# Optimization experiments

Hardware: AMD Instinct MI355X
Metric: run time of the kernel (lower is better)

Reference implementation:

```python
import jax, jax.numpy as jnp
import numpy as np

N = 100000   # nodes
E = 640000   # edges
D = 128      # hidden/in channels
G = 64       # graphs in batch
L = 3        # GCN layers (n_layers - 1)
EPS = 1e-5   # batchnorm eps


def _bn(h, gamma, beta):
    # BatchNorm1d in train mode: biased variance over the node axis
    m = h.mean(axis=0)
    v = h.var(axis=0)
    return (h - m) * jax.lax.rsqrt(v + EPS) * gamma + beta


def setup_inputs() -> dict:
    key = jax.random.key(0)
    ks = jax.random.split(key, 20)
    s = 1.0 / np.sqrt(D)
    inp = {
        "x": jax.random.normal(ks[0], (N, D), jnp.float32),
        "edge_index": jax.random.randint(ks[1], (2, E), 0, N, dtype=jnp.int64),
        "batch": jnp.sort(jax.random.randint(ks[2], (N,), 0, G, dtype=jnp.int64)),
        # encoder MLP (2 layers, batchnorm+relu between)
        "enc_W1": jax.random.normal(ks[3], (D, D), jnp.float32) * s,
        "enc_b1": jnp.zeros((D,), jnp.float32),
        "enc_g": jnp.ones((D,), jnp.float32),
        "enc_be": jnp.zeros((D,), jnp.float32),
        "enc_W2": jax.random.normal(ks[4], (D, D), jnp.float32) * s,
        "enc_b2": jnp.zeros((D,), jnp.float32),
        # stacked GCN layer params
        "conv_W": jax.random.normal(ks[5], (L, D, D), jnp.float32) * s,
        "conv_b": jnp.zeros((L, D), jnp.float32),
        "bn_g": jnp.ones((L, D), jnp.float32),
        "bn_b": jnp.zeros((L, D), jnp.float32),
        # MLPReadout: 128 -> 64 -> 32 -> 1
        "ro_W1": jax.random.normal(ks[6], (D, D // 2), jnp.float32) * s,
        "ro_b1": jnp.zeros((D // 2,), jnp.float32),
        "ro_W2": jax.random.normal(ks[7], (D // 2, D // 4), jnp.float32) * (1.0 / np.sqrt(D // 2)),
        "ro_b2": jnp.zeros((D // 4,), jnp.float32),
        "ro_W3": jax.random.normal(ks[8], (D // 4, 1), jnp.float32) * (1.0 / np.sqrt(D // 4)),
        "ro_b3": jnp.zeros((1,), jnp.float32),
    }
    return inp


def reference(x, edge_index, batch, enc_W1, enc_b1, enc_g, enc_be, enc_W2, enc_b2,
              conv_W, conv_b, bn_g, bn_b, ro_W1, ro_b1, ro_W2, ro_b2, ro_W3, ro_b3):
    src, dst = edge_index[0], edge_index[1]

    # gcn_norm (add_self_loops=False): deg from target column, sym normalization
    deg = jax.ops.segment_sum(jnp.ones((E,), x.dtype), dst, num_segments=N)
    dinv = jnp.where(deg > 0, jax.lax.rsqrt(jnp.maximum(deg, 1.0)), 0.0)
    norm = (dinv[src] * dinv[dst])[:, None]  # [E,1]

    # encoder MLP: Linear -> BN -> ReLU -> Linear
    h = jax.nn.relu(_bn(x @ enc_W1 + enc_b1, enc_g, enc_be))
    h = h @ enc_W2 + enc_b2

    # stacked GCN layers with BN + ReLU + residual
    for l in range(L):
        hw = h @ conv_W[l]                         # [N,D]
        agg = jax.ops.segment_sum(hw[src] * norm, dst, num_segments=N)
        agg = agg + conv_b[l]
        h = h + jax.nn.relu(_bn(agg, bn_g[l], bn_b[l]))

    # scatter-sum pooling per graph
    hg = jax.ops.segment_sum(h, batch, num_segments=G)  # [G,D]

    # MLP readout
    y = jax.nn.relu(hg @ ro_W1 + ro_b1)
    y = jax.nn.relu(y @ ro_W2 + ro_b2)
    y = y @ ro_W3 + ro_b3
    return y
```

## Files before the change

kernel.cpp:

```cpp
#include <hip/hip_runtime.h>
#include <hip/hip_bf16.h>

#define NN 100000
#define NE 640000
#define DD 128
#define NG 64
#define NL 3
#define BN_EPS 1e-5f

typedef unsigned short u16;
typedef unsigned int u32;
typedef __attribute__((ext_vector_type(8))) short short8;
typedef __attribute__((ext_vector_type(4))) float f32x4;

__device__ __forceinline__ void atomAddG(float* p, float v) { unsafeAtomicAdd(p, v); }

__device__ __forceinline__ float bf_lo(u32 u) { return __uint_as_float(u << 16); }
__device__ __forceinline__ float bf_hi(u32 u) { return __uint_as_float(u & 0xffff0000u); }
__device__ __forceinline__ float bfs(short s) { return __uint_as_float(((u32)(u16)s) << 16); }
__device__ __forceinline__ u16 bfb(float f) {
    __hip_bfloat16 b = __float2bfloat16(f);
    return *(u16*)&b;
}
__device__ __forceinline__ u32 pk(float a, float b) {
    return (u32)bfb(a) | ((u32)bfb(b) << 16);
}

__global__ void k_degI(const int* __restrict__ dst, int* __restrict__ degI) {
    int e = blockIdx.x * 256 + threadIdx.x;
    if (e < NE) atomicAdd(&degI[dst[e]], 1);
}

__global__ void k_dinv(const int* __restrict__ degI, float* __restrict__ dinv) {
    int i = blockIdx.x * 256 + threadIdx.x;
    if (i < NN) { int d = degI[i]; dinv[i] = d > 0 ? rsqrtf((float)d) : 0.f; }
}

__global__ void k_scan1(const int* __restrict__ degI, int* __restrict__ offs, int* __restrict__ bsum) {
    __shared__ int ls[256];
    int t = threadIdx.x;
    int i = blockIdx.x * 256 + t;
    int v = (i < NN) ? degI[i] : 0;
    ls[t] = v;
    __syncthreads();
    for (int off = 1; off < 256; off <<= 1) {
        int u = (t >= off) ? ls[t - off] : 0;
        __syncthreads();
        ls[t] += u;
        __syncthreads();
    }
    if (i < NN) offs[i] = ls[t] - v;
    if (t == 255) bsum[blockIdx.x] = ls[255];
}

__global__ void k_scan2(int* __restrict__ bsum, int nb) {
    __shared__ int ls[512];
    int t = threadIdx.x;
    int v = (t < nb) ? bsum[t] : 0;
    ls[t] = v;
    __syncthreads();
    for (int off = 1; off < 512; off <<= 1) {
        int u = (t >= off) ? ls[t - off] : 0;
        __syncthreads();
        ls[t] += u;
        __syncthreads();
    }
    if (t < nb) bsum[t] = ls[t] - v;
}

__global__ void k_scan3(int* __restrict__ offs, const int* __restrict__ bsum) {
    int i = blockIdx.x * 256 + threadIdx.x;
    if (i < NN) offs[i] += bsum[blockIdx.x];
    if (i == 0) offs[NN] = NE;
}

__global__ void k_place(const int* __restrict__ src, const int* __restrict__ dst,
                        const int* __restrict__ offs, int* __restrict__ cur,
                        u32* __restrict__ eIdx) {
    int e = blockIdx.x * 256 + threadIdx.x;
    if (e < NE) {
        int d = dst[e];
        int pos = offs[d] + atomicAdd(&cur[d], 1);
        eIdx[pos] = (u32)src[e];
    }
}

__global__ void k_prepW(const float* __restrict__ W1, const float* __restrict__ W2,
                        const float* __restrict__ CW, u16* __restrict__ wtb) {
    int m = blockIdx.x >> 3;
    const float* src = (m == 0) ? W1 : (m == 1) ? W2 : CW + (size_t)(m - 2) * 16384;
    u16* dst = wtb + (size_t)m * 16384;
    int base = (blockIdx.x & 7) * 2048 + threadIdx.x;
#pragma unroll
    for (int i = 0; i < 8; ++i) {
        int idx = base + i * 256;
        int k = idx >> 7, n = idx & 127;
        dst[n * 128 + k] = bfb(src[idx]);
    }
}

template <int MODE>
__global__ __launch_bounds__(256) void k_mm(
    const void* __restrict__ Av, const u16* __restrict__ Wt,
    const float* __restrict__ bias, const float* __restrict__ scl, const float* __restrict__ shf,
    const float* __restrict__ dinv,
    u16* __restrict__ Cb, float* __restrict__ Cf,
    float* __restrict__ sSum, float* __restrict__ sSq)
{
    __shared__ float lC[64 * 128];
    int tid = threadIdx.x;
    int l = tid & 63, w = tid >> 6;
    int lr = l & 15, lg = l >> 4;
    int wcol = (w & 1) * 64, wrow = (w >> 1) * 32;

    short8 Bf[4][4];
#pragma unroll
    for (int ct = 0; ct < 4; ++ct)
#pragma unroll
        for (int ks = 0; ks < 4; ++ks)
            Bf[ct][ks] = *(const short8*)(Wt + (size_t)(wcol + ct * 16 + lr) * 128 + ks * 32 + lg * 8);

    f32x4 acc[2][4];
#pragma unroll
    for (int rg = 0; rg < 2; ++rg)
#pragma unroll
        for (int ct = 0; ct < 4; ++ct)
            acc[rg][ct] = (f32x4){0.f, 0.f, 0.f, 0.f};

    int rbase = blockIdx.x * 64 + wrow;
#pragma unroll
    for (int rg = 0; rg < 2; ++rg) {
        int row = rbase + rg * 16 + lr;
        row = min(row, NN - 1);
        short8 Af[4];
        if (MODE == 1) {
            const float* af = (const float*)Av + (size_t)row * 128 + lg * 8;
#pragma unroll
            for (int ks = 0; ks < 4; ++ks) {
                float4 v0 = *(const float4*)(af + ks * 32);
                float4 v1 = *(const float4*)(af + ks * 32 + 4);
                short8 o;
                o[0] = (short)bfb(v0.x); o[1] = (short)bfb(v0.y);
                o[2] = (short)bfb(v0.z); o[3] = (short)bfb(v0.w);
                o[4] = (short)bfb(v1.x); o[5] = (short)bfb(v1.y);
                o[6] = (short)bfb(v1.z); o[7] = (short)bfb(v1.w);
                Af[ks] = o;
            }
        } else {
            const u16* ap = (const u16*)Av + (size_t)row * 128 + lg * 8;
#pragma unroll
            for (int ks = 0; ks < 4; ++ks) Af[ks] = *(const short8*)(ap + ks * 32);
            if (MODE == 2) {
#pragma unroll
                for (int ks = 0; ks < 4; ++ks) {
                    int cb = ks * 32 + lg * 8;
                    float4 s0 = *(const float4*)(scl + cb), s1 = *(const float4*)(scl + cb + 4);
                    float4 f0 = *(const float4*)(shf + cb), f1 = *(const float4*)(shf + cb + 4);
                    short8 a = Af[ks], o;
                    o[0] = (short)bfb(fmaxf(0.f, bfs(a[0]) * s0.x + f0.x));
                    o[1] = (short)bfb(fmaxf(0.f, bfs(a[1]) * s0.y + f0.y));
                    o[2] = (short)bfb(fmaxf(0.f, bfs(a[2]) * s0.z + f0.z));
                    o[3] = (short)bfb(fmaxf(0.f, bfs(a[3]) * s0.w + f0.w));
                    o[4] = (short)bfb(fmaxf(0.f, bfs(a[4]) * s1.x + f1.x));
                    o[5] = (short)bfb(fmaxf(0.f, bfs(a[5]) * s1.y + f1.y));
                    o[6] = (short)bfb(fmaxf(0.f, bfs(a[6]) * s1.z + f1.z));
                    o[7] = (short)bfb(fmaxf(0.f, bfs(a[7]) * s1.w + f1.w));
                    Af[ks] = o;
                }
            }
        }
#pragma unroll
        for (int ks = 0; ks < 4; ++ks)
#pragma unroll
            for (int ct = 0; ct < 4; ++ct)
                acc[rg][ct] = __builtin_amdgcn_mfma_f32_16x16x32_bf16(Af[ks], Bf[ct][ks], acc[rg][ct], 0, 0, 0);
    }

    if (MODE == 2) {
#pragma unroll
        for (int ct = 0; ct < 4; ++ct) {
            float bc = bias[wcol + ct * 16 + lr];
#pragma unroll
            for (int rg = 0; rg < 2; ++rg)
#pragma unroll
                for (int j = 0; j < 4; ++j) acc[rg][ct][j] += bc;
        }
    }

#pragma unroll
    for (int rg = 0; rg < 2; ++rg)
#pragma unroll
        for (int ct = 0; ct < 4; ++ct)
#pragma unroll
            for (int j = 0; j < 4; ++j)
                lC[(wrow + rg * 16 + lg * 4 + j) * 128 + wcol + ct * 16 + lr] = acc[rg][ct][j];
    __syncthreads();

    float cs[4] = {0.f, 0.f, 0.f, 0.f}, cq[4] = {0.f, 0.f, 0.f, 0.f};
#pragma unroll
    for (int i = 0; i < 8; ++i) {
        int eidx = i * 1024 + tid * 4;
        int lrow = eidx >> 7;
        int col = eidx & 127;
        int grow = blockIdx.x * 64 + lrow;
        if (grow < NN) {
            float4 v = *(float4*)(lC + eidx);
            if (MODE == 0) {
                float dd = dinv[grow];
                v.x *= dd; v.y *= dd; v.z *= dd; v.w *= dd;
            }
            uint2 o = make_uint2(pk(v.x, v.y), pk(v.z, v.w));
            if (MODE == 0) {
                u32* Cs = (u32*)Cb;
                *(uint2*)(Cs + (size_t)grow * 64 + (col >> 1)) = o;
            } else {
                *(uint2*)(Cb + (size_t)grow * 128 + col) = o;
            }
            if (MODE == 2) *(float4*)(Cf + (size_t)grow * 128 + col) = v;
            if (MODE == 1) {
                cs[0] += v.x; cs[1] += v.y; cs[2] += v.z; cs[3] += v.w;
                cq[0] += v.x * v.x; cq[1] += v.y * v.y; cq[2] += v.z * v.z; cq[3] += v.w * v.w;
            }
        }
    }

    if (MODE == 1) {
        __syncthreads();
        int g = tid >> 5, c0 = (tid & 31) * 4;
#pragma unroll
        for (int cc = 0; cc < 4; ++cc) {
            lC[g * 128 + c0 + cc] = cs[cc];
            lC[1024 + g * 128 + c0 + cc] = cq[cc];
        }
        __syncthreads();
        if (tid < 128) {
            float s = 0.f, q = 0.f;
#pragma unroll
            for (int g2 = 0; g2 < 8; ++g2) { s += lC[g2 * 128 + tid]; q += lC[1024 + g2 * 128 + tid]; }
            atomAddG(&sSum[tid], s);
            atomAddG(&sSq[tid], q);
        }
    }
}

__global__ void k_bnfinal(const float* __restrict__ sSum, const float* __restrict__ sSq,
                          const float* __restrict__ g, const float* __restrict__ be,
                          float* __restrict__ scl, float* __restrict__ shf) {
    int c = threadIdx.x;
    float m = sSum[c] * (1.0f / NN);
    float v = sSq[c] * (1.0f / NN) - m * m;
    float s = g[c] * rsqrtf(v + BN_EPS);
    scl[c] = s;
    shf[c] = be[c] - m * s;
}

__global__ __launch_bounds__(256) void k_agg(
    const u32* __restrict__ hwb,
    const u32* __restrict__ eIdx, const int* __restrict__ offs,
    const float* __restrict__ dinv,
    u32* __restrict__ aggb, float* __restrict__ sSum, float* __restrict__ sSq)
{
    int tid = threadIdx.x;
    int lane = tid & 63;
    int wav = tid >> 6;
    int gw = blockIdx.x * 4 + wav;
    int nw = gridDim.x * 4;
    float sx0 = 0.f, sx1 = 0.f, sq0 = 0.f, sq1 = 0.f;

    for (int d0 = gw * 2; d0 < NN; d0 += nw * 2) {
        int a0 = offs[d0], a1 = offs[d0 + 1], a2 = offs[d0 + 2];
        int len0 = a1 - a0, len1 = a2 - a1;
        int m0 = max(len0 - 1, 0), m1 = max(len1 - 1, 0);
        float x0 = 0.f, y0 = 0.f, x1 = 0.f, y1 = 0.f;
        int mx = max(len0, len1);
        for (int jb = 0; jb < mx; jb += 8) {
            u32 i0[8], i1[8];
#pragma unroll
            for (int q = 0; q < 8; ++q) {
                i0[q] = eIdx[min(a0 + min(jb + q, m0), NE - 1)];
                i1[q] = eIdx[min(a1 + min(jb + q, m1), NE - 1)];
            }
            u32 u0[8], u1[8];
#pragma unroll
            for (int q = 0; q < 8; ++q) {
                u0[q] = hwb[(size_t)i0[q] * 64 + lane];
                u1[q] = hwb[(size_t)i1[q] * 64 + lane];
            }
#pragma unroll
            for (int q = 0; q < 8; ++q) {
                bool v0 = (jb + q) < len0, v1 = (jb + q) < len1;
                x0 += v0 ? bf_lo(u0[q]) : 0.f;
                y0 += v0 ? bf_hi(u0[q]) : 0.f;
                x1 += v1 ? bf_lo(u1[q]) : 0.f;
                y1 += v1 ? bf_hi(u1[q]) : 0.f;
            }
        }
        float dd0 = dinv[d0], dd1 = dinv[d0 + 1];
        x0 *= dd0; y0 *= dd0; x1 *= dd1; y1 *= dd1;
        aggb[(size_t)d0 * 64 + lane] = pk(x0, y0);
        aggb[(size_t)(d0 + 1) * 64 + lane] = pk(x1, y1);
        sx0 += x0 + x1; sx1 += y0 + y1;
        sq0 += x0 * x0 + x1 * x1; sq1 += y0 * y0 + y1 * y1;
    }

    __shared__ float ls[512], lq[512];
    ls[wav * 128 + lane * 2] = sx0;
    ls[wav * 128 + lane * 2 + 1] = sx1;
    lq[wav * 128 + lane * 2] = sq0;
    lq[wav * 128 + lane * 2 + 1] = sq1;
    __syncthreads();
    if (tid < 128) {
        float s = ls[tid] + ls[tid + 128] + ls[tid + 256] + ls[tid + 384];
        float q = lq[tid] + lq[tid + 128] + lq[tid + 256] + lq[tid + 384];
        atomAddG(&sSum[tid], s);
        atomAddG(&sSq[tid], q);
    }
}

__global__ __launch_bounds__(256) void k_update(
    float* __restrict__ h, const u32* __restrict__ aggb,
    const float* __restrict__ scl, const float* __restrict__ shf,
    u32* __restrict__ hb)
{
    int i = blockIdx.x * 256 + threadIdx.x;
    int c0 = (i * 4) & 127;
    uint2 a = *(const uint2*)(aggb + (size_t)i * 2);
    float4 hv = *(float4*)(h + (size_t)i * 4);
    float4 sv = *(const float4*)(scl + c0);
    float4 fv = *(const float4*)(shf + c0);
    hv.x += fmaxf(0.f, bf_lo(a.x) * sv.x + fv.x);
    hv.y += fmaxf(0.f, bf_hi(a.x) * sv.y + fv.y);
    hv.z += fmaxf(0.f, bf_lo(a.y) * sv.z + fv.z);
    hv.w += fmaxf(0.f, bf_hi(a.y) * sv.w + fv.w);
    *(float4*)(h + (size_t)i * 4) = hv;
    *(uint2*)(hb + (size_t)i * 2) = make_uint2(pk(hv.x, hv.y), pk(hv.z, hv.w));
}

__global__ __launch_bounds__(256) void k_pool(
    const float* __restrict__ h, const u32* __restrict__ aggb,
    const float* __restrict__ scl, const float* __restrict__ shf,
    const int* __restrict__ batch, float* __restrict__ hg)
{
    __shared__ float lsum[128];
    int tid = threadIdx.x;
    int c = tid & 127, half = tid >> 7;
    float sc = scl[c], sf = shf[c];
    int r0 = blockIdx.x * 64;
    int rend = min(r0 + 64, NN);
    int b0 = batch[r0], b1 = batch[rend - 1];

    if (b0 == b1) {
        float acc = 0.f;
        for (int r = r0 + half; r < rend; r += 2) {
            u32 a = aggb[(size_t)r * 64 + (c >> 1)];
            float av = (c & 1) ? bf_hi(a) : bf_lo(a);
            acc += h[(size_t)r * 128 + c] + fmaxf(0.f, av * sc + sf);
        }
        if (half) lsum[c] = acc;
        __syncthreads();
        if (!half) atomAddG(&hg[b0 * DD + c], acc + lsum[c]);
    } else {
        float acc = 0.f;
        int cur = batch[r0 + half];
        for (int r = r0 + half; r < rend; r += 2) {
            int b = batch[r];
            if (b != cur) { atomAddG(&hg[cur * DD + c], acc); acc = 0.f; cur = b; }
            u32 a = aggb[(size_t)r * 64 + (c >> 1)];
            float av = (c & 1) ? bf_hi(a) : bf_lo(a);
            acc += h[(size_t)r * 128 + c] + fmaxf(0.f, av * sc + sf);
        }
        atomAddG(&hg[cur * DD + c], acc);
    }
}

__global__ __launch_bounds__(128) void k_readout(
    const float* __restrict__ hg,
    const float* __restrict__ W1, const float* __restrict__ b1,
    const float* __restrict__ W2, const float* __restrict__ b2,
    const float* __restrict__ W3, const float* __restrict__ b3,
    float* __restrict__ out) {
    __shared__ float a0[128], a1[64], a2[32];
    int g = blockIdx.x, t = threadIdx.x;
    a0[t] = hg[g * DD + t];
    __syncthreads();
    if (t < 64) {
        float s = b1[t];
        for (int k = 0; k < 128; ++k) s += a0[k] * W1[k * 64 + t];
        a1[t] = fmaxf(s, 0.f);
    }
    __syncthreads();
    if (t < 32) {
        float s = b2[t];
        for (int k = 0; k < 64; ++k) s += a1[k] * W2[k * 32 + t];
        a2[t] = fmaxf(s, 0.f);
    }
    __syncthreads();
    if (t == 0) {
        float s = b3[0];
        for (int k = 0; k < 32; ++k) s += a2[k] * W3[k];
        out[g] = s;
    }
}

extern "C" void kernel_launch(void* const* d_in, const int* in_sizes, int n_in,
                              void* d_out, int out_size, void* d_ws, size_t ws_size,
                              hipStream_t stream) {
    const float* x      = (const float*)d_in[0];
    const int*   ei     = (const int*)d_in[1];
    const int*   batch  = (const int*)d_in[2];
    const float* enc_W1 = (const float*)d_in[3];
    const float* enc_g  = (const float*)d_in[5];
    const float* enc_be = (const float*)d_in[6];
    const float* enc_W2 = (const float*)d_in[7];
    const float* enc_b2 = (const float*)d_in[8];
    const float* conv_W = (const float*)d_in[9];
    const float* bn_g   = (const float*)d_in[11];
    const float* bn_b   = (const float*)d_in[12];
    const float* ro_W1  = (const float*)d_in[13];
    const float* ro_b1  = (const float*)d_in[14];
    const float* ro_W2  = (const float*)d_in[15];
    const float* ro_b2  = (const float*)d_in[16];
    const float* ro_W3  = (const float*)d_in[17];
    const float* ro_b3  = (const float*)d_in[18];

    const int* srcI = ei;
    const int* dstI = ei + NE;

    float* ws   = (float*)d_ws;
    float* h    = ws;
    u32*   aggb = (u32*)(ws + 12800000);
    u32*   hb   = (u32*)(ws + 19200000);
    u32*   t1b  = (u32*)(ws + 25600000);
    u16*   wtb  = (u16*)(ws + 32000000);
    float* dinv = ws + 32050000;
    float* sSum = ws + 32150000;
    float* sSq  = sSum + 128;
    float* scl  = sSum + 256;
    float* shf  = sSum + 384;
    float* hg   = ws + 32150512;
    int*   offs = (int*)(ws + 32160000);
    int*   degI = (int*)(ws + 32270000);
    int*   bsum = (int*)(ws + 32370000);
    u32*   eIdx = (u32*)(ws + 32380000);

    u16* tb16 = (u16*)aggb;

    k_prepW<<<40, 256, 0, stream>>>(enc_W1, enc_W2, conv_W, wtb);

    hipMemsetAsync(degI, 0, NN * sizeof(int), stream);
    k_degI<<<2500, 256, 0, stream>>>(dstI, degI);
    k_dinv<<<391, 256, 0, stream>>>(degI, dinv);
    k_scan1<<<391, 256, 0, stream>>>(degI, offs, bsum);
    k_scan2<<<1, 512, 0, stream>>>(bsum, 391);
    k_scan3<<<391, 256, 0, stream>>>(offs, bsum);
    hipMemsetAsync(degI, 0, NN * sizeof(int), stream);
    k_place<<<2500, 256, 0, stream>>>(srcI, dstI, offs, degI, eIdx);

    hipMemsetAsync(sSum, 0, 256 * sizeof(float), stream);
    k_mm<1><<<1563, 256, 0, stream>>>(x, wtb, nullptr, nullptr, nullptr, nullptr, tb16, nullptr, sSum, sSq);
    k_bnfinal<<<1, 128, 0, stream>>>(sSum, sSq, enc_g, enc_be, scl, shf);
    k_mm<2><<<1563, 256, 0, stream>>>(tb16, wtb + 16384, enc_b2, scl, shf, nullptr, (u16*)hb, h, nullptr, nullptr);

    for (int l = 0; l < NL; ++l) {
        k_mm<0><<<1563, 256, 0, stream>>>((const u16*)hb, wtb + (size_t)(2 + l) * 16384,
                                          nullptr, nullptr, nullptr, dinv, (u16*)t1b, nullptr, nullptr, nullptr);
        hipMemsetAsync(sSum, 0, 256 * sizeof(float), stream);
        k_agg<<<2048, 256, 0, stream>>>(t1b, eIdx, offs, dinv, aggb, sSum, sSq);
        k_bnfinal<<<1, 128, 0, stream>>>(sSum, sSq, bn_g + l * DD, bn_b + l * DD, scl, shf);
        if (l < NL - 1)
            k_update<<<12500, 256, 0, stream>>>(h, aggb, scl, shf, hb);
    }

    hipMemsetAsync(hg, 0, NG * DD * sizeof(float), stream);
    k_pool<<<1563, 256, 0, stream>>>(h, aggb, scl, shf, batch, hg);
    k_readout<<<NG, 128, 0, stream>>>(hg, ro_W1, ro_b1, ro_W2, ro_b2, ro_W3, ro_b3, (float*)d_out);
}
```

Baseline: 534.5 us.

## Store transformed features in column-sliced layout and aggregate per slice for cache locality

The matmul output feeding aggregation is now stored as 8 column slices of 32 bytes per node, each slice contiguous over all nodes. The aggregation kernel assigns each block one slice and one contiguous range of destinations. Each wave gathers 8 edges in parallel, with 8 lanes reading one node's 32-byte slice, then reduces across lanes with shuffles. The intent is a smaller per-slice working set (about 3.2 MB) that fits in cache for the random gathers. The cost is narrower 32-byte gathers, extra shuffle reductions, and eight times as many index loads per edge.

```diff
diff --git a/kernel.cpp b/kernel.cpp
--- a/kernel.cpp
+++ b/kernel.cpp
@@ -211,8 +211,9 @@
             }
             uint2 o = make_uint2(pk(v.x, v.y), pk(v.z, v.w));
             if (MODE == 0) {
+                int cu = col >> 1, sl = cu >> 3, c = cu & 7;
                 u32* Cs = (u32*)Cb;
-                *(uint2*)(Cs + (size_t)grow * 64 + (col >> 1)) = o;
+                *(uint2*)(Cs + (size_t)sl * (NN * 8) + (size_t)grow * 8 + c) = o;
             } else {
                 *(uint2*)(Cb + (size_t)grow * 128 + col) = o;
             }
@@ -254,66 +255,79 @@
     shf[c] = be[c] - m * s;
 }
 
-__global__ __launch_bounds__(256) void k_agg(
-    const u32* __restrict__ hwb,
+__global__ __launch_bounds__(256) void k_aggs(
+    const u32* __restrict__ t1s,
     const u32* __restrict__ eIdx, const int* __restrict__ offs,
     const float* __restrict__ dinv,
     u32* __restrict__ aggb, float* __restrict__ sSum, float* __restrict__ sSq)
 {
     int tid = threadIdx.x;
-    int lane = tid & 63;
-    int wav = tid >> 6;
-    int gw = blockIdx.x * 4 + wav;
-    int nw = gridDim.x * 4;
+    int slice = blockIdx.x & 7;
+    int blk = blockIdx.x >> 3;
+    int lane = tid & 63, wav = tid >> 6;
+    int g = lane >> 3, cc = lane & 7;
+
+    const u32* hsl = t1s + (size_t)slice * (NN * 8);
+    const int DPB = (NN + 255) / 256;
+    int base = blk * DPB;
+    int dend = min(base + DPB, NN);
+
     float sx0 = 0.f, sx1 = 0.f, sq0 = 0.f, sq1 = 0.f;
 
-    for (int d0 = gw * 2; d0 < NN; d0 += nw * 2) {
-        int a0 = offs[d0], a1 = offs[d0 + 1], a2 = offs[d0 + 2];
-        int len0 = a1 - a0, len1 = a2 - a1;
+    for (int d0 = base + wav * 2; d0 < dend; d0 += 8) {
+        int d1 = d0 + 1;
+        bool has1 = d1 < dend;
+        int js0 = offs[d0], je0 = offs[d0 + 1];
+        int js1 = has1 ? offs[d1] : js0;
+        int je1 = has1 ? offs[d1 + 1] : js1;
+        int len0 = je0 - js0, len1 = je1 - js1;
         int m0 = max(len0 - 1, 0), m1 = max(len1 - 1, 0);
+        int mx = max(len0, len1);
         float x0 = 0.f, y0 = 0.f, x1 = 0.f, y1 = 0.f;
-        int mx = max(len0, len1);
         for (int jb = 0; jb < mx; jb += 8) {
-            u32 i0[8], i1[8];
-#pragma unroll
-            for (int q = 0; q < 8; ++q) {
-                i0[q] = eIdx[min(a0 + min(jb + q, m0), NE - 1)];
-                i1[q] = eIdx[min(a1 + min(jb + q, m1), NE - 1)];
-            }
-            u32 u0[8], u1[8];
-#pragma unroll
-            for (int q = 0; q < 8; ++q) {
-                u0[q] = hwb[(size_t)i0[q] * 64 + lane];
-                u1[q] = hwb[(size_t)i1[q] * 64 + lane];
-            }
-#pragma unroll
-            for (int q = 0; q < 8; ++q) {
-                bool v0 = (jb + q) < len0, v1 = (jb + q) < len1;
-                x0 += v0 ? bf_lo(u0[q]) : 0.f;
-                y0 += v0 ? bf_hi(u0[q]) : 0.f;
-                x1 += v1 ? bf_lo(u1[q]) : 0.f;
-                y1 += v1 ? bf_hi(u1[q]) : 0.f;
-            }
-        }
-        float dd0 = dinv[d0], dd1 = dinv[d0 + 1];
-        x0 *= dd0; y0 *= dd0; x1 *= dd1; y1 *= dd1;
-        aggb[(size_t)d0 * 64 + lane] = pk(x0, y0);
-        aggb[(size_t)(d0 + 1) * 64 + lane] = pk(x1, y1);
-        sx0 += x0 + x1; sx1 += y0 + y1;
-        sq0 += x0 * x0 + x1 * x1; sq1 += y0 * y0 + y1 * y1;
-    }
-
-    __shared__ float ls[512], lq[512];
-    ls[wav * 128 + lane * 2] = sx0;
-    ls[wav * 128 + lane * 2 + 1] = sx1;
-    lq[wav * 128 + lane * 2] = sq0;
-    lq[wav * 128 + lane * 2 + 1] = sq1;
-    __syncthreads();
-    if (tid < 128) {
-        float s = ls[tid] + ls[tid + 128] + ls[tid + 256] + ls[tid + 384];
-        float q = lq[tid] + lq[tid + 128] + lq[tid + 256] + lq[tid + 384];
-        atomAddG(&sSum[tid], s);
-        atomAddG(&sSq[tid], q);
+            int e0 = min(jb + g, m0), e1 = min(jb + g, m1);
+            u32 r0 = eIdx[min(js0 + e0, NE - 1)];
+            u32 r1 = eIdx[min(js1 + e1, NE - 1)];
+            u32 u0 = hsl[(size_t)r0 * 8 + cc];
+            u32 u1 = hsl[(size_t)r1 * 8 + cc];
+            bool v0 = (jb + g) < len0, v1 = (jb + g) < len1;
+            x0 += v0 ? bf_lo(u0) : 0.f;
+            y0 += v0 ? bf_hi(u0) : 0.f;
+            x1 += v1 ? bf_lo(u1) : 0.f;
+            y1 += v1 ? bf_hi(u1) : 0.f;
+        }
+#pragma unroll
+        for (int off = 8; off < 64; off <<= 1) {
+            x0 += __shfl_xor(x0, off);
+            y0 += __shfl_xor(y0, off);
+            x1 += __shfl_xor(x1, off);
+            y1 += __shfl_xor(y1, off);
+        }
+        if (g == 0) {
+            float dd0 = dinv[d0];
+            float vx = x0 * dd0, vy = y0 * dd0;
+            aggb[(size_t)d0 * 64 + slice * 8 + cc] = pk(vx, vy);
+            sx0 += vx; sx1 += vy; sq0 += vx * vx; sq1 += vy * vy;
+            if (has1) {
+                float dd1 = dinv[d1];
+                float wx = x1 * dd1, wy = y1 * dd1;
+                aggb[(size_t)d1 * 64 + slice * 8 + cc] = pk(wx, wy);
+                sx0 += wx; sx1 += wy; sq0 += wx * wx; sq1 += wy * wy;
+            }
+        }
+    }
+
+    __shared__ float red[4][4][8];
+    if (lane < 8) { red[0][wav][lane] = sx0; red[1][wav][lane] = sx1; red[2][wav][lane] = sq0; red[3][wav][lane] = sq1; }
+    __syncthreads();
+    if (tid < 8) {
+        float a0 = red[0][0][tid] + red[0][1][tid] + red[0][2][tid] + red[0][3][tid];
+        float a1 = red[1][0][tid] + red[1][1][tid] + red[1][2][tid] + red[1][3][tid];
+        float b0 = red[2][0][tid] + red[2][1][tid] + red[2][2][tid] + red[2][3][tid];
+        float b1 = red[3][0][tid] + red[3][1][tid] + red[3][2][tid] + red[3][3][tid];
+        int c2 = (slice * 8 + tid) * 2;
+        atomAddG(&sSum[c2], a0);  atomAddG(&sSum[c2 + 1], a1);
+        atomAddG(&sSq[c2], b0);   atomAddG(&sSq[c2 + 1], b1);
     }
 }
 
@@ -430,7 +444,7 @@
     float* h    = ws;
     u32*   aggb = (u32*)(ws + 12800000);
     u32*   hb   = (u32*)(ws + 19200000);
-    u32*   t1b  = (u32*)(ws + 25600000);
+    u32*   t1s  = (u32*)(ws + 25600000);
     u16*   wtb  = (u16*)(ws + 32000000);
     float* dinv = ws + 32050000;
     float* sSum = ws + 32150000;
@@ -463,9 +477,9 @@
 
     for (int l = 0; l < NL; ++l) {
         k_mm<0><<<1563, 256, 0, stream>>>((const u16*)hb, wtb + (size_t)(2 + l) * 16384,
-                                          nullptr, nullptr, nullptr, dinv, (u16*)t1b, nullptr, nullptr, nullptr);
+                                          nullptr, nullptr, nullptr, dinv, (u16*)t1s, nullptr, nullptr, nullptr);
         hipMemsetAsync(sSum, 0, 256 * sizeof(float), stream);
-        k_agg<<<2048, 256, 0, stream>>>(t1b, eIdx, offs, dinv, aggb, sSum, sSq);
+        k_aggs<<<2048, 256, 0, stream>>>(t1s, eIdx, offs, dinv, aggb, sSum, sSq);
         k_bnfinal<<<1, 128, 0, stream>>>(sSum, sSq, bn_g + l * DD, bn_b + l * DD, scl, shf);
         if (l < NL - 1)
             k_update<<<12500, 256, 0, stream>>>(h, aggb, scl, shf, hb);
```

Result: slower. 685.1 us (+28.2%).

## Fuse residual BN-ReLU update into next GCN layer's matmul prologue

Applied to the files above, without the earlier changes.

Removes the separate k_update kernel and the bf16 copy of h (hb). Each later GCN matmul now loads h and the aggregated features, applies the BN-scale/shift, ReLU and residual add, writes h back, and stages the fp32 rows in XOR-swizzled shared memory to feed the MFMA. The encoder's second matmul now writes only fp32 h, and the first GCN layer reads fp32 h directly. This saves one kernel launch and a round trip of h per layer. In exchange the matmul reads fp32 instead of bf16 and adds an extra barrier.

```diff
diff --git a/kernel.cpp b/kernel.cpp
--- a/kernel.cpp
+++ b/kernel.cpp
@@ -103,8 +103,8 @@
 __global__ __launch_bounds__(256) void k_mm(
     const void* __restrict__ Av, const u16* __restrict__ Wt,
     const float* __restrict__ bias, const float* __restrict__ scl, const float* __restrict__ shf,
-    const float* __restrict__ dinv,
-    u16* __restrict__ Cb, float* __restrict__ Cf,
+    const float* __restrict__ dinv, const u32* __restrict__ agg,
+    float* __restrict__ hmut, u16* __restrict__ Cb,
     float* __restrict__ sSum, float* __restrict__ sSq)
 {
     __shared__ float lC[64 * 128];
@@ -120,6 +120,29 @@
         for (int ks = 0; ks < 4; ++ks)
             Bf[ct][ks] = *(const short8*)(Wt + (size_t)(wcol + ct * 16 + lr) * 128 + ks * 32 + lg * 8);
 
+    if (MODE == 3) {
+#pragma unroll
+        for (int i = 0; i < 8; ++i) {
+            int eidx = i * 1024 + tid * 4;
+            int lrow = eidx >> 7, col = eidx & 127;
+            int grow = blockIdx.x * 64 + lrow;
+            float4 v = make_float4(0.f, 0.f, 0.f, 0.f);
+            if (grow < NN) {
+                v = *(const float4*)((const float*)Av + (size_t)grow * 128 + col);
+                uint2 a2 = *(const uint2*)(agg + (size_t)grow * 64 + (col >> 1));
+                float4 sv = *(const float4*)(scl + col);
+                float4 fv = *(const float4*)(shf + col);
+                v.x += fmaxf(0.f, bf_lo(a2.x) * sv.x + fv.x);
+                v.y += fmaxf(0.f, bf_hi(a2.x) * sv.y + fv.y);
+                v.z += fmaxf(0.f, bf_lo(a2.y) * sv.z + fv.z);
+                v.w += fmaxf(0.f, bf_hi(a2.y) * sv.w + fv.w);
+                *(float4*)(hmut + (size_t)grow * 128 + col) = v;
+            }
+            *(float4*)(lC + lrow * 128 + (col ^ ((lrow & 7) << 2))) = v;
+        }
+        __syncthreads();
+    }
+
     f32x4 acc[2][4];
 #pragma unroll
     for (int rg = 0; rg < 2; ++rg)
@@ -130,10 +153,45 @@
     int rbase = blockIdx.x * 64 + wrow;
 #pragma unroll
     for (int rg = 0; rg < 2; ++rg) {
-        int row = rbase + rg * 16 + lr;
-        row = min(row, NN - 1);
+        int row0 = rbase + rg * 16 + lr;
+        int row = min(row0, NN - 1);
         short8 Af[4];
-        if (MODE == 1) {
+        if (MODE == 3) {
+            int lrl = wrow + rg * 16 + lr;
+            int s = (lrl & 7) << 2;
+            const float* lp = lC + lrl * 128;
+#pragma unroll
+            for (int ks = 0; ks < 4; ++ks) {
+                int c0 = ks * 32 + lg * 8;
+                float4 v0 = *(const float4*)(lp + (c0 ^ s));
+                float4 v1 = *(const float4*)(lp + ((c0 + 4) ^ s));
+                short8 o;
+                o[0] = (short)bfb(v0.x); o[1] = (short)bfb(v0.y);
+                o[2] = (short)bfb(v0.z); o[3] = (short)bfb(v0.w);
+                o[4] = (short)bfb(v1.x); o[5] = (short)bfb(v1.y);
+                o[6] = (short)bfb(v1.z); o[7] = (short)bfb(v1.w);
+                Af[ks] = o;
+            }
+        } else if (MODE == 2) {
+            const u16* ap = (const u16*)Av + (size_t)row * 128 + lg * 8;
+#pragma unroll
+            for (int ks = 0; ks < 4; ++ks) {
+                short8 a = *(const short8*)(ap + ks * 32);
+                int cb = ks * 32 + lg * 8;
+                float4 s0 = *(const float4*)(scl + cb), s1 = *(const float4*)(scl + cb + 4);
+                float4 f0 = *(const float4*)(shf + cb), f1 = *(const float4*)(shf + cb + 4);
+                short8 o;
+                o[0] = (short)bfb(fmaxf(0.f, bfs(a[0]) * s0.x + f0.x));
+                o[1] = (short)bfb(fmaxf(0.f, bfs(a[1]) * s0.y + f0.y));
+                o[2] = (short)bfb(fmaxf(0.f, bfs(a[2]) * s0.z + f0.z));
+                o[3] = (short)bfb(fmaxf(0.f, bfs(a[3]) * s0.w + f0.w));
+                o[4] = (short)bfb(fmaxf(0.f, bfs(a[4]) * s1.x + f1.x));
+                o[5] = (short)bfb(fmaxf(0.f, bfs(a[5]) * s1.y + f1.y));
+                o[6] = (short)bfb(fmaxf(0.f, bfs(a[6]) * s1.z + f1.z));
+                o[7] = (short)bfb(fmaxf(0.f, bfs(a[7]) * s1.w + f1.w));
+                Af[ks] = o;
+            }
+        } else {
             const float* af = (const float*)Av + (size_t)row * 128 + lg * 8;
 #pragma unroll
             for (int ks = 0; ks < 4; ++ks) {
@@ -146,28 +204,6 @@
                 o[6] = (short)bfb(v1.z); o[7] = (short)bfb(v1.w);
                 Af[ks] = o;
             }
-        } else {
-            const u16* ap = (const u16*)Av + (size_t)row * 128 + lg * 8;
-#pragma unroll
-            for (int ks = 0; ks < 4; ++ks) Af[ks] = *(const short8*)(ap + ks * 32);
-            if (MODE == 2) {
-#pragma unroll
-                for (int ks = 0; ks < 4; ++ks) {
-                    int cb = ks * 32 + lg * 8;
-                    float4 s0 = *(const float4*)(scl + cb), s1 = *(const float4*)(scl + cb + 4);
-                    float4 f0 = *(const float4*)(shf + cb), f1 = *(const float4*)(shf + cb + 4);
-                    short8 a = Af[ks], o;
-                    o[0] = (short)bfb(fmaxf(0.f, bfs(a[0]) * s0.x + f0.x));
-                    o[1] = (short)bfb(fmaxf(0.f, bfs(a[1]) * s0.y + f0.y));
-                    o[2] = (short)bfb(fmaxf(0.f, bfs(a[2]) * s0.z + f0.z));
-                    o[3] = (short)bfb(fmaxf(0.f, bfs(a[3]) * s0.w + f0.w));
-                    o[4] = (short)bfb(fmaxf(0.f, bfs(a[4]) * s1.x + f1.x));
-                    o[5] = (short)bfb(fmaxf(0.f, bfs(a[5]) * s1.y + f1.y));
-                    o[6] = (short)bfb(fmaxf(0.f, bfs(a[6]) * s1.z + f1.z));
-                    o[7] = (short)bfb(fmaxf(0.f, bfs(a[7]) * s1.w + f1.w));
-                    Af[ks] = o;
-                }
-            }
         }
 #pragma unroll
         for (int ks = 0; ks < 4; ++ks)
@@ -186,6 +222,8 @@
                 for (int j = 0; j < 4; ++j) acc[rg][ct][j] += bc;
         }
     }
+
+    if (MODE == 3) __syncthreads();
 
 #pragma unroll
     for (int rg = 0; rg < 2; ++rg)
@@ -205,19 +243,17 @@
         int grow = blockIdx.x * 64 + lrow;
         if (grow < NN) {
             float4 v = *(float4*)(lC + eidx);
-            if (MODE == 0) {
+            if (MODE == 3 || MODE == 4) {
                 float dd = dinv[grow];
                 v.x *= dd; v.y *= dd; v.z *= dd; v.w *= dd;
-            }
-            uint2 o = make_uint2(pk(v.x, v.y), pk(v.z, v.w));
-            if (MODE == 0) {
                 u32* Cs = (u32*)Cb;
-                *(uint2*)(Cs + (size_t)grow * 64 + (col >> 1)) = o;
+                *(uint2*)(Cs + (size_t)grow * 64 + (col >> 1)) =
+                    make_uint2(pk(v.x, v.y), pk(v.z, v.w));
+            } else if (MODE == 2) {
+                *(float4*)(hmut + (size_t)grow * 128 + col) = v;
             } else {
-                *(uint2*)(Cb + (size_t)grow * 128 + col) = o;
-            }
-            if (MODE == 2) *(float4*)(Cf + (size_t)grow * 128 + col) = v;
-            if (MODE == 1) {
+                *(uint2*)(Cb + (size_t)grow * 128 + col) =
+                    make_uint2(pk(v.x, v.y), pk(v.z, v.w));
                 cs[0] += v.x; cs[1] += v.y; cs[2] += v.z; cs[3] += v.w;
                 cq[0] += v.x * v.x; cq[1] += v.y * v.y; cq[2] += v.z * v.z; cq[3] += v.w * v.w;
             }
@@ -315,25 +351,6 @@
         atomAddG(&sSum[tid], s);
         atomAddG(&sSq[tid], q);
     }
-}
-
-__global__ __launch_bounds__(256) void k_update(
-    float* __restrict__ h, const u32* __restrict__ aggb,
-    const float* __restrict__ scl, const float* __restrict__ shf,
-    u32* __restrict__ hb)
-{
-    int i = blockIdx.x * 256 + threadIdx.x;
-    int c0 = (i * 4) & 127;
-    uint2 a = *(const uint2*)(aggb + (size_t)i * 2);
-    float4 hv = *(float4*)(h + (size_t)i * 4);
-    float4 sv = *(const float4*)(scl + c0);
-    float4 fv = *(const float4*)(shf + c0);
-    hv.x += fmaxf(0.f, bf_lo(a.x) * sv.x + fv.x);
-    hv.y += fmaxf(0.f, bf_hi(a.x) * sv.y + fv.y);
-    hv.z += fmaxf(0.f, bf_lo(a.y) * sv.z + fv.z);
-    hv.w += fmaxf(0.f, bf_hi(a.y) * sv.w + fv.w);
-    *(float4*)(h + (size_t)i * 4) = hv;
-    *(uint2*)(hb + (size_t)i * 2) = make_uint2(pk(hv.x, hv.y), pk(hv.z, hv.w));
 }
 
 __global__ __launch_bounds__(256) void k_pool(
@@ -429,19 +446,18 @@
     float* ws   = (float*)d_ws;
     float* h    = ws;
     u32*   aggb = (u32*)(ws + 12800000);
-    u32*   hb   = (u32*)(ws + 19200000);
-    u32*   t1b  = (u32*)(ws + 25600000);
-    u16*   wtb  = (u16*)(ws + 32000000);
-    float* dinv = ws + 32050000;
-    float* sSum = ws + 32150000;
+    u32*   t1b  = (u32*)(ws + 19200000);
+    u16*   wtb  = (u16*)(ws + 25600000);
+    float* dinv = ws + 25700000;
+    float* sSum = ws + 25801000;
     float* sSq  = sSum + 128;
     float* scl  = sSum + 256;
     float* shf  = sSum + 384;
-    float* hg   = ws + 32150512;
-    int*   offs = (int*)(ws + 32160000);
-    int*   degI = (int*)(ws + 32270000);
-    int*   bsum = (int*)(ws + 32370000);
-    u32*   eIdx = (u32*)(ws + 32380000);
+    float* hg   = ws + 25802000;
+    int*   offs = (int*)(ws + 25811000);
+    int*   degI = (int*)(ws + 25912000);
+    int*   bsum = (int*)(ws + 26013000);
+    u32*   eIdx = (u32*)(ws + 26014000);
 
     u16* tb16 = (u16*)aggb;
 
@@ -457,18 +473,24 @@
     k_place<<<2500, 256, 0, stream>>>(srcI, dstI, offs, degI, eIdx);
 
     hipMemsetAsync(sSum, 0, 256 * sizeof(float), stream);
-    k_mm<1><<<1563, 256, 0, stream>>>(x, wtb, nullptr, nullptr, nullptr, nullptr, tb16, nullptr, sSum, sSq);
+    k_mm<1><<<1563, 256, 0, stream>>>(x, wtb, nullptr, nullptr, nullptr, nullptr, nullptr,
+                                      nullptr, tb16, sSum, sSq);
     k_bnfinal<<<1, 128, 0, stream>>>(sSum, sSq, enc_g, enc_be, scl, shf);
-    k_mm<2><<<1563, 256, 0, stream>>>(tb16, wtb + 16384, enc_b2, scl, shf, nullptr, (u16*)hb, h, nullptr, nullptr);
-
-    for (int l = 0; l < NL; ++l) {
-        k_mm<0><<<1563, 256, 0, stream>>>((const u16*)hb, wtb + (size_t)(2 + l) * 16384,
-                                          nullptr, nullptr, nullptr, dinv, (u16*)t1b, nullptr, nullptr, nullptr);
+    k_mm<2><<<1563, 256, 0, stream>>>(tb16, wtb + 16384, enc_b2, scl, shf, nullptr, nullptr,
+                                      h, nullptr, nullptr, nullptr);
+
+    k_mm<4><<<1563, 256, 0, stream>>>(h, wtb + 2 * 16384, nullptr, nullptr, nullptr, dinv, nullptr,
+                                      nullptr, (u16*)t1b, nullptr, nullptr);
+    hipMemsetAsync(sSum, 0, 256 * sizeof(float), stream);
+    k_agg<<<2048, 256, 0, stream>>>(t1b, eIdx, offs, dinv, aggb, sSum, sSq);
+    k_bnfinal<<<1, 128, 0, stream>>>(sSum, sSq, bn_g, bn_b, scl, shf);
+
+    for (int l = 1; l < NL; ++l) {
+        k_mm<3><<<1563, 256, 0, stream>>>(h, wtb + (size_t)(2 + l) * 16384, nullptr, scl, shf,
+                                          dinv, aggb, h, (u16*)t1b, nullptr, nullptr);
         hipMemsetAsync(sSum, 0, 256 * sizeof(float), stream);
         k_agg<<<2048, 256, 0, stream>>>(t1b, eIdx, offs, dinv, aggb, sSum, sSq);
         k_bnfinal<<<1, 128, 0, stream>>>(sSum, sSq, bn_g + l * DD, bn_b + l * DD, scl, shf);
-        if (l < NL - 1)
-            k_update<<<12500, 256, 0, stream>>>(h, aggb, scl, shf, hb);
     }
 
     hipMemsetAsync(hg, 0, NG * DD * sizeof(float), stream);
```

Result: slower. 577.8 us (+8.1%).
